# Kernel optimization log

Measured on AMD Instinct MI355X. Metric: run time of the kernel, lower is better.

The kernel has to match this reference:

```python
import jax, jax.numpy as jnp
import numpy as np

B, T, C = 4, 2048, 1024
H = 16
D = C // H  # head_dim = 64


def setup_inputs() -> dict:
    key = jax.random.key(0)
    k1, k2, k3 = jax.random.split(key, 3)
    x = jax.random.normal(k1, (B, T, C), dtype=jnp.float32)
    w_qkv = jax.random.normal(k2, (C, 3 * C), dtype=jnp.float32) * (C ** -0.5)
    b_qkv = jnp.zeros((3 * C,), dtype=jnp.float32)
    w_proj = jax.random.normal(k3, (C, C), dtype=jnp.float32) * (C ** -0.5)
    b_proj = jnp.zeros((C,), dtype=jnp.float32)
    return {"x": x, "w_qkv": w_qkv, "b_qkv": b_qkv, "w_proj": w_proj, "b_proj": b_proj}


def reference(x, w_qkv, b_qkv, w_proj, b_proj):
    # qkv projection: (B,T,C) -> (B,T,3,H,D) -> q,k,v each (B,H,T,D)
    qkv = (x @ w_qkv + b_qkv).reshape(B, T, 3, H, D)
    q, k, v = jnp.moveaxis(qkv, 2, 0)           # each (B, T, H, D)
    q = q.transpose(0, 2, 1, 3)                 # (B, H, T, D)
    k = k.transpose(0, 2, 1, 3)
    v = v.transpose(0, 2, 1, 3)

    scale = 1.0 / jnp.sqrt(jnp.float32(D))
    attn = jnp.einsum('bhqd,bhkd->bhqk', q, k) * scale  # (B,H,T,T)
    causal = jnp.tril(jnp.ones((T, T), dtype=bool))
    attn = jnp.where(causal[None, None], attn, -jnp.inf)
    attn = jax.nn.softmax(attn, axis=-1)
    # dropout p=0.0 (eval mode) -> identity
    out = jnp.einsum('bhqk,bhkd->bhqd', attn, v)        # (B,H,T,D)
    out = out.transpose(0, 2, 1, 3).reshape(B, T, C)
    return out @ w_proj + b_proj
```

## Files before the change

### kernel.cpp

```cpp
#include <hip/hip_runtime.h>
#include <hip/hip_bf16.h>


#define Bsz 4
#define Tsz 2048
#define Csz 1024
#define Hn  16
#define Dh  64

typedef unsigned short u16;
typedef __attribute__((ext_vector_type(8))) short bf16x8;
typedef __attribute__((ext_vector_type(4))) float f32x4;
typedef __attribute__((ext_vector_type(4))) unsigned int u32x4;
typedef __attribute__((ext_vector_type(2))) unsigned int u32x2;

__device__ __forceinline__ u16 f2b(float f) {
  __hip_bfloat16 h = __float2bfloat16(f);
  return *reinterpret_cast<u16*>(&h);
}

__device__ __forceinline__ unsigned pk2(float lo, float hi) {
  return __builtin_amdgcn_perm(__float_as_uint(hi) + 0x8000u,
                               __float_as_uint(lo) + 0x8000u, 0x07060302u);
}

#if __has_builtin(__builtin_amdgcn_exp2f)
#define EX2(x) __builtin_amdgcn_exp2f(x)
#else
#define EX2(x) exp2f(x)
#endif

__device__ __forceinline__ void gld_lds16(const void* g, void* lds) {
  __builtin_amdgcn_global_load_lds(
      (const __attribute__((address_space(1))) unsigned int*)g,
      (__attribute__((address_space(3))) unsigned int*)lds, 16, 0, 0);
}

__global__ __launch_bounds__(256) void cvt_f32_bf16(const float* __restrict__ in,
                                                    u16* __restrict__ out) {
  size_t i = ((size_t)blockIdx.x * 256 + threadIdx.x) * 8;
  f32x4 a = *(const f32x4*)(in + i);
  f32x4 b = *(const f32x4*)(in + i + 4);
  u16 r[8];
#pragma unroll
  for (int j = 0; j < 4; ++j) { r[j] = f2b(a[j]); r[4 + j] = f2b(b[j]); }
  *(u32x4*)(out + i) = *(const u32x4*)r;
}

__global__ __launch_bounds__(256) void cvt_transpose(const float* __restrict__ in,
                                                     u16* __restrict__ out,
                                                     int R, int C) {
  __shared__ u16 tile[64 * 66];
  const int r0 = blockIdx.x * 64, c0 = blockIdx.y * 64;
  const int tid = threadIdx.x;
#pragma unroll
  for (int i = 0; i < 16; ++i) {
    int idx = i * 256 + tid;
    int r = idx >> 6, c = idx & 63;
    tile[r * 66 + c] = f2b(in[(size_t)(r0 + r) * C + (c0 + c)]);
  }
  __syncthreads();
#pragma unroll
  for (int i = 0; i < 16; ++i) {
    int idx = i * 256 + tid;
    int c = idx >> 6, r = idx & 63;
    out[(size_t)(c0 + c) * R + (r0 + r)] = tile[r * 66 + c];
  }
}

__device__ __forceinline__ void gemm_tile_acc(const u16* __restrict__ A,
                                              const u16* __restrict__ Bt,
                                              int m0, int n0,
                                              u16* Alds, u16* Blds,
                                              f32x4 acc[4][4]) {
  const int tid = threadIdx.x;
  const int w = tid >> 6, lane = tid & 63;
  const int wm = w & 1, wn = w >> 1;
  const int col = lane & 15, quad = lane >> 4;
  const int lrow = lane >> 2;
  const int kseg = (lane & 3) * 8;
#pragma unroll
  for (int mt = 0; mt < 4; ++mt)
#pragma unroll
    for (int nt = 0; nt < 4; ++nt)
      acc[mt][nt] = (f32x4){0.f, 0.f, 0.f, 0.f};

  for (int k0 = 0; k0 < 1024; k0 += 32) {
    __syncthreads();
#pragma unroll
    for (int g = 0; g < 2; ++g) {
      int grp = w * 2 + g;
      gld_lds16(A + (size_t)(m0 + grp * 16 + lrow) * 1024 + k0 + kseg,
                (char*)Alds + grp * 1024);
      gld_lds16(Bt + (size_t)(n0 + grp * 16 + lrow) * 1024 + k0 + kseg,
                (char*)Blds + grp * 1024);
    }
    __syncthreads();
    bf16x8 af[4], bfr[4];
#pragma unroll
    for (int mt = 0; mt < 4; ++mt)
      af[mt] = *(const bf16x8*)(Alds + (wm * 64 + mt * 16 + col) * 32 + quad * 8);
#pragma unroll
    for (int nt = 0; nt < 4; ++nt)
      bfr[nt] = *(const bf16x8*)(Blds + (wn * 64 + nt * 16 + col) * 32 + quad * 8);
#pragma unroll
    for (int mt = 0; mt < 4; ++mt)
#pragma unroll
      for (int nt = 0; nt < 4; ++nt)
        acc[mt][nt] = __builtin_amdgcn_mfma_f32_16x16x32_bf16(af[mt], bfr[nt],
                                                              acc[mt][nt], 0, 0, 0);
  }
}

__global__ __launch_bounds__(256) void gemm_qkv(const u16* __restrict__ X,
                                                const u16* __restrict__ WT,
                                                const float* __restrict__ bias,
                                                u16* __restrict__ Q,
                                                u16* __restrict__ Kc,
                                                u16* __restrict__ Vt) {
  __shared__ __align__(16) u16 Alds[128 * 32];
  __shared__ __align__(16) u16 Blds[128 * 32];
  f32x4 acc[4][4];
  const int m0 = blockIdx.x * 128, n0 = blockIdx.y * 128;
  gemm_tile_acc(X, WT, m0, n0, Alds, Blds, acc);

  const float qscale = 0.18033688011112042f;
  const int tid = threadIdx.x;
  const int w = tid >> 6, lane = tid & 63;
  const int wm = w & 1, wn = w >> 1;
  const int col = lane & 15, quad = lane >> 4;
#pragma unroll
  for (int mt = 0; mt < 4; ++mt)
#pragma unroll
    for (int nt = 0; nt < 4; ++nt) {
      int n = n0 + wn * 64 + nt * 16 + col;
      int s = n >> 10, hh = (n >> 6) & (Hn - 1), d = n & 63;
      int mBase = m0 + wm * 64 + mt * 16 + quad * 4;
      int b = mBase >> 11, t0 = mBase & (Tsz - 1);
      if (s == 2) {
        u16 vals[4];
#pragma unroll
        for (int r = 0; r < 4; ++r) vals[r] = f2b(acc[mt][nt][r] + bias[n]);
        *(u32x2*)(Vt + ((size_t)(b * Hn + hh) * Dh + d) * Tsz + t0) =
            *(const u32x2*)vals;
      } else {
        const float scl = (s == 0) ? qscale : 1.f;
        u16* dst = (s == 0) ? Q : Kc;
#pragma unroll
        for (int r = 0; r < 4; ++r)
          dst[((size_t)(b * Hn + hh) * Tsz + (t0 + r)) * Dh + d] =
              f2b((acc[mt][nt][r] + bias[n]) * scl);
      }
    }
}

__global__ __launch_bounds__(256) void gemm_proj(const u16* __restrict__ O,
                                                 const u16* __restrict__ WT,
                                                 const float* __restrict__ bias,
                                                 float* __restrict__ out) {
  __shared__ __align__(16) u16 Alds[128 * 32];
  __shared__ __align__(16) u16 Blds[128 * 32];
  f32x4 acc[4][4];
  const int m0 = blockIdx.x * 128, n0 = blockIdx.y * 128;
  gemm_tile_acc(O, WT, m0, n0, Alds, Blds, acc);

  const int tid = threadIdx.x;
  const int w = tid >> 6, lane = tid & 63;
  const int wm = w & 1, wn = w >> 1;
  const int col = lane & 15, quad = lane >> 4;
#pragma unroll
  for (int mt = 0; mt < 4; ++mt)
#pragma unroll
    for (int nt = 0; nt < 4; ++nt)
#pragma unroll
      for (int r = 0; r < 4; ++r) {
        int m = m0 + wm * 64 + mt * 16 + quad * 4 + r;
        int n = n0 + wn * 64 + nt * 16 + col;
        out[(size_t)m * Csz + n] = acc[mt][nt][r] + bias[n];
      }
}

__device__ __forceinline__ void attn_tile_stage(
    const u16* __restrict__ Kc, const u16* __restrict__ Vc,
    const bf16x8* aq, f32x4* oacc, float* lsum,
    bool domask, int rel, int qg, int col, int quad, int off0, int off1) {
  f32x4 sacc[4];
#pragma unroll
  for (int kt = 0; kt < 4; ++kt) sacc[kt] = (f32x4){0.f, 0.f, 0.f, 0.f};
#pragma unroll
  for (int ks = 0; ks < 2; ++ks)
#pragma unroll
    for (int kt = 0; kt < 4; ++kt) {
      bf16x8 bk = *(const bf16x8*)(&Kc[(kt * 16 + col) * 64 + (ks ? off1 : off0)]);
      sacc[kt] = __builtin_amdgcn_mfma_f32_16x16x32_bf16(bk, aq[ks],
                                                         sacc[kt], 0, 0, 0);
    }

  float e[4][4];
  if (domask) {
#pragma unroll
    for (int kt = 0; kt < 4; ++kt)
#pragma unroll
      for (int r = 0; r < 4; ++r) {
        int kl = rel + kt * 16 + quad * 4 + r;
        float p = (kl > qg) ? 0.f : EX2(sacc[kt][r]);
        lsum[kt] += p;
        e[kt][r] = p;
      }
  } else {
#pragma unroll
    for (int kt = 0; kt < 4; ++kt)
#pragma unroll
      for (int r = 0; r < 4; ++r) {
        float p = EX2(sacc[kt][r]);
        lsum[kt] += p;
        e[kt][r] = p;
      }
  }

#pragma unroll
  for (int ksg = 0; ksg < 2; ++ksg) {
    unsigned w00 = pk2(e[2 * ksg][0], e[2 * ksg][1]);
    unsigned w01 = pk2(e[2 * ksg][2], e[2 * ksg][3]);
    unsigned w10 = pk2(e[2 * ksg + 1][0], e[2 * ksg + 1][1]);
    unsigned w11 = pk2(e[2 * ksg + 1][2], e[2 * ksg + 1][3]);
    auto ra = __builtin_amdgcn_permlane32_swap(w00, w10, false, false);
    auto rb = __builtin_amdgcn_permlane32_swap(w01, w11, false, false);
    auto sa = __builtin_amdgcn_permlane16_swap(ra[0], ra[1], false, false);
    auto sb = __builtin_amdgcn_permlane16_swap(rb[0], rb[1], false, false);
    union { unsigned u[4]; bf16x8 v; } pf;
    pf.u[0] = sa[0]; pf.u[1] = sb[0]; pf.u[2] = sa[1]; pf.u[3] = sb[1];
#pragma unroll
    for (int dt = 0; dt < 4; ++dt) {
      bf16x8 bv = *(const bf16x8*)(&Vc[(dt * 16 + col) * 64 + (ksg ? off1 : off0)]);
      oacc[dt] = __builtin_amdgcn_mfma_f32_16x16x32_bf16(bv, pf.v,
                                                         oacc[dt], 0, 0, 0);
    }
  }
}

__global__ __launch_bounds__(512, 4) void attn(const u16* __restrict__ Q,
                                               const u16* __restrict__ Kg,
                                               const u16* __restrict__ Vt,
                                               u16* __restrict__ O) {
  __shared__ __align__(16) u16 Ks[3][64 * 64];
  __shared__ __align__(16) u16 Vs[3][64 * 64];

  const int d0 = blockIdx.x;
  const int xcd = d0 & 7;
  const int idx = d0 >> 3;
  const int bh = ((idx & 7) << 3) | xcd;
  const int a = idx >> 3;
  const int qlo = a, qhi = 15 - a;
  const int h = bh & (Hn - 1), b = bh >> 4;

  const int tid = threadIdx.x, w = tid >> 6, lane = tid & 63;
  const int col = lane & 15, quad = lane >> 4;
  const int qbl = qlo << 7, qbh = qhi << 7;

  const u16* Kbase = Kg + (size_t)bh * Tsz * Dh;
  const u16* Vbase = Vt + (size_t)bh * Dh * Tsz;

  const int trow = tid >> 3;
  const int xseg = ((tid & 7) ^ (trow & 7)) * 8;
  const size_t koff = (size_t)trow * 64 + xseg;
  const size_t voff = (size_t)trow * Tsz + xseg;
  const int swz = col & 7;
  const int off0 = ((0 + quad) ^ swz) << 3;
  const int off1 = ((4 + quad) ^ swz) << 3;

  bf16x8 aq_hi[2], aq_lo[2];
  {
    const u16* Qh = Q + ((size_t)bh * Tsz + qbh) * Dh;
    const u16* Ql = Q + ((size_t)bh * Tsz + qbl) * Dh;
#pragma unroll
    for (int ks = 0; ks < 2; ++ks) {
      aq_hi[ks] = *(const bf16x8*)(Qh + (size_t)(w * 16 + col) * Dh + ks * 32 + quad * 8);
      aq_lo[ks] = *(const bf16x8*)(Ql + (size_t)(w * 16 + col) * Dh + ks * 32 + quad * 8);
    }
  }
  asm volatile("s_waitcnt vmcnt(0)" ::: "memory");

  const int nst = 2 * qhi + 2;
  gld_lds16(Kbase + koff, &Ks[0][w * 512]);
  gld_lds16(Vbase + voff, &Vs[0][w * 512]);
  gld_lds16(Kbase + 4096 + koff, &Ks[1][w * 512]);
  gld_lds16(Vbase + 64 + voff, &Vs[1][w * 512]);

  f32x4 oacc_hi[4], oacc_lo[4];
#pragma unroll
  for (int dt = 0; dt < 4; ++dt) {
    oacc_hi[dt] = (f32x4){0.f, 0.f, 0.f, 0.f};
    oacc_lo[dt] = (f32x4){0.f, 0.f, 0.f, 0.f};
  }
  float lsum_hi[4] = {0.f, 0.f, 0.f, 0.f};
  float lsum_lo[4] = {0.f, 0.f, 0.f, 0.f};

  const u16* kdma = Kbase + 2 * 4096 + koff;
  const u16* vdma = Vbase + 2 * 64 + voff;

  const int qg = w * 16 + col;
  const int wge4 = (w >= 4) ? 1 : 0;
  const int smask_hi = 2 * qhi + wge4;
  const int smask_lo = 2 * qlo + wge4;
  const int lo_end = 2 * qlo + 1 + wge4;
  const int hi2 = 2 * qhi, lo2 = 2 * qlo;

  int cur = 0;
  for (int s = 0; s < nst; ++s) {
    if (s + 1 < nst) {
      asm volatile("s_waitcnt vmcnt(2)" ::: "memory");
    } else {
      asm volatile("s_waitcnt vmcnt(0)" ::: "memory");
    }
    __builtin_amdgcn_s_barrier();
    __builtin_amdgcn_sched_barrier(0);
    if (s + 2 < nst) {
      int pf = cur + 2; if (pf >= 3) pf -= 3;
      gld_lds16(kdma, &Ks[pf][w * 512]);
      gld_lds16(vdma, &Vs[pf][w * 512]);
      kdma += 4096;
      vdma += 64;
    }
    const u16* Kc = &Ks[cur][0];
    const u16* Vc = &Vs[cur][0];

    if (w >= 4 || s < nst - 1)
      attn_tile_stage(Kc, Vc, aq_hi, oacc_hi, lsum_hi,
                      s >= smask_hi, (s - hi2) * 64, qg, col, quad, off0, off1);
    if (s < lo_end)
      attn_tile_stage(Kc, Vc, aq_lo, oacc_lo, lsum_lo,
                      s >= smask_lo, (s - lo2) * 64, qg, col, quad, off0, off1);

    cur += 1; if (cur >= 3) cur = 0;
  }

  float vh = (lsum_hi[0] + lsum_hi[1]) + (lsum_hi[2] + lsum_hi[3]);
  vh += __shfl_xor(vh, 16);
  vh += __shfl_xor(vh, 32);
  const float invh = 1.0f / vh;
  float vl = (lsum_lo[0] + lsum_lo[1]) + (lsum_lo[2] + lsum_lo[3]);
  vl += __shfl_xor(vl, 16);
  vl += __shfl_xor(vl, 32);
  const float invl = 1.0f / vl;

  const int rgh = qbh + w * 16 + col;
  const int rgl = qbl + w * 16 + col;
  u16* OrowH = O + (((size_t)b * Tsz + rgh) * Hn + h) * Dh;
  u16* OrowL = O + (((size_t)b * Tsz + rgl) * Hn + h) * Dh;
#pragma unroll
  for (int dt = 0; dt < 4; ++dt) {
    u16 vh4[4], vl4[4];
#pragma unroll
    for (int r = 0; r < 4; ++r) {
      vh4[r] = f2b(oacc_hi[dt][r] * invh);
      vl4[r] = f2b(oacc_lo[dt][r] * invl);
    }
    *(u32x2*)(OrowH + dt * 16 + quad * 4) = *(const u32x2*)vh4;
    *(u32x2*)(OrowL + dt * 16 + quad * 4) = *(const u32x2*)vl4;
  }
}

extern "C" void kernel_launch(void* const* d_in, const int* in_sizes, int n_in,
                              void* d_out, int out_size, void* d_ws, size_t ws_size,
                              hipStream_t stream) {
  const float* x      = (const float*)d_in[0];
  const float* w_qkv  = (const float*)d_in[1];
  const float* b_qkv  = (const float*)d_in[2];
  const float* w_proj = (const float*)d_in[3];
  const float* b_proj = (const float*)d_in[4];
  float* out = (float*)d_out;

  u16* Xb     = (u16*)d_ws;
  u16* WqkvT  = Xb + (size_t)8192 * 1024;
  u16* WprojT = WqkvT + (size_t)3072 * 1024;
  u16* Qb     = WprojT + (size_t)1024 * 1024;
  u16* Kb     = Qb + (size_t)8192 * 1024;
  u16* Ob     = Kb + (size_t)8192 * 1024;
  u16* Vtb    = (u16*)d_out;

  cvt_f32_bf16<<<4096, 256, 0, stream>>>(x, Xb);
  cvt_transpose<<<dim3(16, 48), 256, 0, stream>>>(w_qkv, WqkvT, 1024, 3072);
  cvt_transpose<<<dim3(16, 16), 256, 0, stream>>>(w_proj, WprojT, 1024, 1024);
  gemm_qkv<<<dim3(64, 24), 256, 0, stream>>>(Xb, WqkvT, b_qkv, Qb, Kb, Vtb);
  attn<<<dim3(512), 512, 0, stream>>>(Qb, Kb, Vtb, Ob);
  gemm_proj<<<dim3(64, 8), 256, 0, stream>>>(Ob, WprojT, b_proj, out);
}
```

Before: 240.5 us.

## Double-buffer GEMM LDS tiles with BK=64 and XOR-swizzled layout

Rewrites the shared GEMM mainloop for the QKV and output projections. The K-step grows from 32 to 64 and the LDS tiles are double-buffered, so global-to-LDS loads for the next tile are issued before computing the current one. Each loop iteration now has one barrier instead of two. An XOR swizzle on the 16-byte segments is meant to avoid LDS bank conflicts on the fragment reads. LDS per block grows to 64 KB and launch bounds ask for 2 blocks per CU, which may limit occupancy or raise register pressure.

New measurement: 249.2 us. +3.6%, slower.

```diff
diff --git a/kernel.cpp b/kernel.cpp
--- a/kernel.cpp
+++ b/kernel.cpp
@@ -71,58 +71,93 @@
 __device__ __forceinline__ void gemm_tile_acc(const u16* __restrict__ A,
                                               const u16* __restrict__ Bt,
                                               int m0, int n0,
-                                              u16* Alds, u16* Blds,
+                                              u16* Als, u16* Bls,
                                               f32x4 acc[4][4]) {
   const int tid = threadIdx.x;
   const int w = tid >> 6, lane = tid & 63;
   const int wm = w & 1, wn = w >> 1;
   const int col = lane & 15, quad = lane >> 4;
-  const int lrow = lane >> 2;
-  const int kseg = (lane & 3) * 8;
 #pragma unroll
   for (int mt = 0; mt < 4; ++mt)
 #pragma unroll
     for (int nt = 0; nt < 4; ++nt)
       acc[mt][nt] = (f32x4){0.f, 0.f, 0.f, 0.f};
 
-  for (int k0 = 0; k0 < 1024; k0 += 32) {
-    __syncthreads();
-#pragma unroll
-    for (int g = 0; g < 2; ++g) {
-      int grp = w * 2 + g;
-      gld_lds16(A + (size_t)(m0 + grp * 16 + lrow) * 1024 + k0 + kseg,
-                (char*)Alds + grp * 1024);
-      gld_lds16(Bt + (size_t)(n0 + grp * 16 + lrow) * 1024 + k0 + kseg,
-                (char*)Blds + grp * 1024);
-    }
-    __syncthreads();
-    bf16x8 af[4], bfr[4];
-#pragma unroll
-    for (int mt = 0; mt < 4; ++mt)
-      af[mt] = *(const bf16x8*)(Alds + (wm * 64 + mt * 16 + col) * 32 + quad * 8);
-#pragma unroll
-    for (int nt = 0; nt < 4; ++nt)
-      bfr[nt] = *(const bf16x8*)(Blds + (wn * 64 + nt * 16 + col) * 32 + quad * 8);
-#pragma unroll
-    for (int mt = 0; mt < 4; ++mt)
-#pragma unroll
-      for (int nt = 0; nt < 4; ++nt)
-        acc[mt][nt] = __builtin_amdgcn_mfma_f32_16x16x32_bf16(af[mt], bfr[nt],
-                                                              acc[mt][nt], 0, 0, 0);
-  }
-}
-
-__global__ __launch_bounds__(256) void gemm_qkv(const u16* __restrict__ X,
-                                                const u16* __restrict__ WT,
-                                                const float* __restrict__ bias,
-                                                u16* __restrict__ Q,
-                                                u16* __restrict__ Kc,
-                                                u16* __restrict__ Vt) {
-  __shared__ __align__(16) u16 Alds[128 * 32];
-  __shared__ __align__(16) u16 Blds[128 * 32];
+  const u16* asrc[4];
+  const u16* bsrc[4];
+#pragma unroll
+  for (int c = 0; c < 4; ++c) {
+    int slot = c * 256 + tid;
+    int trow = slot >> 3, seg = slot & 7;
+    size_t off = (size_t)trow * 1024 + (size_t)((seg ^ (trow & 7)) * 8);
+    asrc[c] = A + (size_t)m0 * 1024 + off;
+    bsrc[c] = Bt + (size_t)n0 * 1024 + off;
+  }
+  const int swz = col & 7;
+  const int o0 = ((0 + quad) ^ swz) * 8;
+  const int o1 = ((4 + quad) ^ swz) * 8;
+
+#pragma unroll
+  for (int c = 0; c < 4; ++c) {
+    gld_lds16(asrc[c], (char*)Als + (size_t)(c * 256 + w * 64) * 16);
+    gld_lds16(bsrc[c], (char*)Bls + (size_t)(c * 256 + w * 64) * 16);
+    asrc[c] += 64; bsrc[c] += 64;
+  }
+
+  const int nkt = 1024 / 64;
+  for (int t = 0; t < nkt; ++t) {
+    asm volatile("s_waitcnt vmcnt(0)" ::: "memory");
+    __builtin_amdgcn_s_barrier();
+    __builtin_amdgcn_sched_barrier(0);
+    const int cur = t & 1;
+    if (t + 1 < nkt) {
+      const int nxt = cur ^ 1;
+      u16* Ad = Als + nxt * 8192;
+      u16* Bd = Bls + nxt * 8192;
+#pragma unroll
+      for (int c = 0; c < 4; ++c) {
+        gld_lds16(asrc[c], (char*)Ad + (size_t)(c * 256 + w * 64) * 16);
+        gld_lds16(bsrc[c], (char*)Bd + (size_t)(c * 256 + w * 64) * 16);
+        asrc[c] += 64; bsrc[c] += 64;
+      }
+    }
+    const u16* Ac = Als + cur * 8192;
+    const u16* Bc = Bls + cur * 8192;
+    bf16x8 af[4][2], bfr[4][2];
+#pragma unroll
+    for (int mt = 0; mt < 4; ++mt) {
+      const u16* r = Ac + (size_t)(wm * 64 + mt * 16 + col) * 64;
+      af[mt][0] = *(const bf16x8*)(r + o0);
+      af[mt][1] = *(const bf16x8*)(r + o1);
+    }
+#pragma unroll
+    for (int nt = 0; nt < 4; ++nt) {
+      const u16* r = Bc + (size_t)(wn * 64 + nt * 16 + col) * 64;
+      bfr[nt][0] = *(const bf16x8*)(r + o0);
+      bfr[nt][1] = *(const bf16x8*)(r + o1);
+    }
+#pragma unroll
+    for (int kk = 0; kk < 2; ++kk)
+#pragma unroll
+      for (int mt = 0; mt < 4; ++mt)
+#pragma unroll
+        for (int nt = 0; nt < 4; ++nt)
+          acc[mt][nt] = __builtin_amdgcn_mfma_f32_16x16x32_bf16(
+              af[mt][kk], bfr[nt][kk], acc[mt][nt], 0, 0, 0);
+  }
+}
+
+__global__ __launch_bounds__(256, 2) void gemm_qkv(const u16* __restrict__ X,
+                                                   const u16* __restrict__ WT,
+                                                   const float* __restrict__ bias,
+                                                   u16* __restrict__ Q,
+                                                   u16* __restrict__ Kc,
+                                                   u16* __restrict__ Vt) {
+  __shared__ __align__(16) u16 Als[2 * 128 * 64];
+  __shared__ __align__(16) u16 Bls[2 * 128 * 64];
   f32x4 acc[4][4];
   const int m0 = blockIdx.x * 128, n0 = blockIdx.y * 128;
-  gemm_tile_acc(X, WT, m0, n0, Alds, Blds, acc);
+  gemm_tile_acc(X, WT, m0, n0, Als, Bls, acc);
 
   const float qscale = 0.18033688011112042f;
   const int tid = threadIdx.x;
@@ -154,15 +189,15 @@
     }
 }
 
-__global__ __launch_bounds__(256) void gemm_proj(const u16* __restrict__ O,
-                                                 const u16* __restrict__ WT,
-                                                 const float* __restrict__ bias,
-                                                 float* __restrict__ out) {
-  __shared__ __align__(16) u16 Alds[128 * 32];
-  __shared__ __align__(16) u16 Blds[128 * 32];
+__global__ __launch_bounds__(256, 2) void gemm_proj(const u16* __restrict__ O,
+                                                    const u16* __restrict__ WT,
+                                                    const float* __restrict__ bias,
+                                                    float* __restrict__ out) {
+  __shared__ __align__(16) u16 Als[2 * 128 * 64];
+  __shared__ __align__(16) u16 Bls[2 * 128 * 64];
   f32x4 acc[4][4];
   const int m0 = blockIdx.x * 128, n0 = blockIdx.y * 128;
-  gemm_tile_acc(O, WT, m0, n0, Alds, Blds, acc);
+  gemm_tile_acc(O, WT, m0, n0, Als, Bls, acc);
 
   const int tid = threadIdx.x;
   const int w = tid >> 6, lane = tid & 63;
```
